# Kernel tuning notes

Measured on AMD Instinct MI355X. Metric: run time of the kernel, lower is better.

## Reference

```python
import jax, jax.numpy as jnp
import numpy as np

CAPACITY_FACTOR = 1.2


def setup_inputs() -> dict:
    key = jax.random.key(0)
    k1, k2, k3 = jax.random.split(key, 3)
    B, S, D, E = 8, 4096, 512, 16
    x = jax.random.normal(k1, (B, S, D), dtype=jnp.float32)
    switch_w = jax.random.normal(k2, (E, D), dtype=jnp.float32) * 0.02
    switch_b = jnp.zeros((E,), dtype=jnp.float32)
    expert_w = jax.random.normal(k3, (E, D, D), dtype=jnp.float32) * 0.02
    expert_b = jnp.zeros((E, D), dtype=jnp.float32)
    return {"x": x, "switch_w": switch_w, "switch_b": switch_b,
            "expert_w": expert_w, "expert_b": expert_b}


def reference(x, switch_w, switch_b, expert_w, expert_b):
    B, S, D = x.shape
    E = switch_w.shape[0]
    N = B * S
    xf = x.reshape(N, D)

    # Router: softmax over experts, top-1 route.
    logits = xf @ switch_w.T + switch_b            # [N, E]
    probs = jax.nn.softmax(logits, axis=-1)
    route_probs = jnp.max(probs, axis=-1)          # [N]
    routes = jnp.argmax(probs, axis=-1)            # [N] int

    # Position of each token within its expert's queue (token order).
    oh = jax.nn.one_hot(routes, E, dtype=jnp.int32)            # [N, E]
    pos = jnp.take_along_axis(jnp.cumsum(oh, axis=0), routes[:, None], axis=1)[:, 0] - 1  # [N]

    capacity = int(CAPACITY_FACTOR * N / E)        # static
    keep = pos < capacity                          # [N] bool; overflow tokens dropped

    # Dispatch: scatter kept tokens into [E, capacity, D] buffer.
    # Out-of-capacity positions are out-of-bounds and dropped by scatter semantics.
    buf = jnp.zeros((E, capacity, D), dtype=xf.dtype).at[routes, pos].set(xf)

    # Per-expert Linear (torch Linear: y = x @ W.T + b), as one grouped GEMM.
    y = jnp.einsum('ecd,efd->ecf', buf, expert_w) + expert_b[:, None, :]  # [E, C, D]

    # Combine: gather expert outputs back; dropped tokens pass through x.
    gathered = y[routes, jnp.minimum(pos, capacity - 1)]       # [N, D]
    out = jnp.where(keep[:, None], gathered, xf) * route_probs[:, None]
    return out.reshape(B, S, D)
```

## Files before the change

### kernel.cpp

```cpp
#include <hip/hip_runtime.h>
#include <math.h>

#define N_TOK 32768
#define DIM   512
#define NEXP  16
#define CAP   2457
#define CAPP  2464
#define NCHUNK 512

typedef __attribute__((ext_vector_type(8))) short   short8;
typedef __attribute__((ext_vector_type(4))) short   short4v;
typedef __attribute__((ext_vector_type(4))) float   floatx4;
typedef __attribute__((ext_vector_type(4))) unsigned uint4v;

__device__ __forceinline__ short f2bf(float f) {
  unsigned u = __builtin_bit_cast(unsigned, f);
  unsigned r = u + 0x7FFFu + ((u >> 16) & 1u);
  return (short)(r >> 16);
}
__device__ __forceinline__ float bf2f(short h) {
  return __builtin_bit_cast(float, ((unsigned)(unsigned short)h) << 16);
}

__device__ __forceinline__ unsigned cvt_pk(float a, float b) {
  unsigned r;
  asm("v_cvt_pk_bf16_f32 %0, %1, %2" : "=v"(r) : "v"(a), "v"(b));
  return r;
}
__device__ __forceinline__ float pklo(unsigned h) {
  return __builtin_bit_cast(float, h << 16);
}
__device__ __forceinline__ float pkhi(unsigned h) {
  return __builtin_bit_cast(float, h & 0xFFFF0000u);
}

#define LGP 17
__global__ __launch_bounds__(256) void router_k(
    const float* __restrict__ x, const float* __restrict__ sw,
    const float* __restrict__ sb, const float* __restrict__ ew,
    int* __restrict__ route, float* __restrict__ prob, int* __restrict__ hist,
    short* __restrict__ x_bf, short* __restrict__ w_bf) {
  __shared__ short swh[16][520];
  __shared__ short swl[16][520];
  __shared__ float lgt[64][LGP];
  __shared__ float sbs[NEXP];

  int tid = threadIdx.x;

  {
    const float4* src = (const float4*)ew;
    uint2* dst = (uint2*)w_bf;
    int base = blockIdx.x * 2048 + tid;
#pragma unroll
    for (int i = 0; i < 8; ++i) {
      float4 f = src[base + i * 256];
      uint2 s;
      s.x = cvt_pk(f.x, f.y);
      s.y = cvt_pk(f.z, f.w);
      dst[base + i * 256] = s;
    }
  }

  {
    int idx = tid;
#pragma unroll
    for (int i = 0; i < 8; ++i, idx += 256) {
      int e = idx >> 7, k4 = idx & 127;
      float4 f = ((const float4*)(sw + e * DIM))[k4];
      unsigned h0 = cvt_pk(f.x, f.y);
      unsigned h1 = cvt_pk(f.z, f.w);
      unsigned l0 = cvt_pk(f.x - pklo(h0), f.y - pkhi(h0));
      unsigned l1 = cvt_pk(f.z - pklo(h1), f.w - pkhi(h1));
      uint2 hv; hv.x = h0; hv.y = h1;
      uint2 lv; lv.x = l0; lv.y = l1;
      *(uint2*)&swh[e][k4 * 4] = hv;
      *(uint2*)&swl[e][k4 * 4] = lv;
    }
  }
  if (tid < NEXP) sbs[tid] = sb[tid];
  __syncthreads();

  int wv = tid >> 6, lane = tid & 63, q = lane >> 4, l16 = lane & 15;
  int row = blockIdx.x * 64 + wv * 16 + l16;
  const float* xr = x + (size_t)row * DIM;
  short* xbr = x_bf + (size_t)row * DIM;

  floatx4 acc = {};
#pragma unroll 4
  for (int kc = 0; kc < 16; ++kc) {
    int k0 = kc * 32 + q * 8;
    float4 f0 = *(const float4*)(xr + k0);
    float4 f1 = *(const float4*)(xr + k0 + 4);
    unsigned h0 = cvt_pk(f0.x, f0.y);
    unsigned h1 = cvt_pk(f0.z, f0.w);
    unsigned h2 = cvt_pk(f1.x, f1.y);
    unsigned h3 = cvt_pk(f1.z, f1.w);
    unsigned l0 = cvt_pk(f0.x - pklo(h0), f0.y - pkhi(h0));
    unsigned l1 = cvt_pk(f0.z - pklo(h1), f0.w - pkhi(h1));
    unsigned l2 = cvt_pk(f1.x - pklo(h2), f1.y - pkhi(h2));
    unsigned l3 = cvt_pk(f1.z - pklo(h3), f1.w - pkhi(h3));
    uint4v hp = {h0, h1, h2, h3};
    uint4v lp = {l0, l1, l2, l3};
    short8 hi = __builtin_bit_cast(short8, hp);
    short8 lo = __builtin_bit_cast(short8, lp);
    *(short8*)(xbr + k0) = hi;
    short8 bh = *(const short8*)&swh[l16][k0];
    short8 bl = *(const short8*)&swl[l16][k0];
    acc = __builtin_amdgcn_mfma_f32_16x16x32_bf16(hi, bh, acc, 0, 0, 0);
    acc = __builtin_amdgcn_mfma_f32_16x16x32_bf16(lo, bh, acc, 0, 0, 0);
    acc = __builtin_amdgcn_mfma_f32_16x16x32_bf16(hi, bl, acc, 0, 0, 0);
  }
#pragma unroll
  for (int r = 0; r < 4; ++r)
    lgt[wv * 16 + q * 4 + r][l16] = acc[r];
  __syncthreads();

  if (tid < 64) {
    int t = blockIdx.x * 64 + tid;
    float lg[NEXP];
#pragma unroll
    for (int e = 0; e < NEXP; ++e) lg[e] = lgt[tid][e] + sbs[e];
    int arg = 0; float mx = lg[0];
#pragma unroll
    for (int e = 1; e < NEXP; ++e)
      if (lg[e] > mx) { mx = lg[e]; arg = e; }
    float s = 0.f;
#pragma unroll
    for (int e = 0; e < NEXP; ++e) s += expf(lg[e] - mx);
    route[t] = arg;
    prob[t]  = 1.0f / s;
#pragma unroll
    for (int e = 0; e < NEXP; ++e) {
      unsigned long long m = __ballot(arg == e);
      if (tid == e) hist[blockIdx.x * NEXP + e] = __popcll(m);
    }
  }
}

__global__ __launch_bounds__(256) void pos_k(
    const int* __restrict__ route, const float* __restrict__ prob,
    const int* __restrict__ hist, const float* __restrict__ x,
    float* __restrict__ out, int* __restrict__ lists,
    int* __restrict__ counts) {
  __shared__ int part[16][NEXP];
  __shared__ int base_s[NEXP];
  __shared__ int wcnt[4][NEXP];
  int tid = threadIdx.x;
  int b = blockIdx.x;
  int c0 = b * 4;
  {
    int g = tid >> 4, e = tid & 15;
    int s = 0;
    for (int c = g; c < c0; c += 16) s += hist[c * NEXP + e];
    part[g][e] = s;
  }
  __syncthreads();
  if (tid < NEXP) {
    int s = 0;
#pragma unroll
    for (int gg = 0; gg < 16; ++gg) s += part[gg][tid];
    base_s[tid] = s;
  }
  int wv = tid >> 6, lane = tid & 63;
  int t = b * 256 + wv * 64 + lane;
  int r = route[t];
  unsigned long long lower = (1ull << lane) - 1ull;
  int rank = 0;
#pragma unroll
  for (int e = 0; e < NEXP; ++e) {
    unsigned long long m = __ballot(r == e);
    if (r == e) rank = __popcll(m & lower);
    if (lane == e) wcnt[wv][e] = __popcll(m);
  }
  __syncthreads();
  int pre = base_s[r];
  for (int w2 = 0; w2 < wv; ++w2) pre += wcnt[w2][r];
  int pos = pre + rank;
  if (pos < CAP) {
    lists[r * CAPP + pos] = t;
  } else {
    float p = prob[t];
    const float4* xr = (const float4*)(x + (size_t)t * DIM);
    float4* o = (float4*)(out + (size_t)t * DIM);
    for (int d = 0; d < DIM / 4; ++d) {
      float4 v = xr[d];
      v.x *= p; v.y *= p; v.z *= p; v.w *= p;
      o[d] = v;
    }
  }
  if (b == 127 && tid < NEXP)
    counts[tid] = base_s[tid] + wcnt[0][tid] + wcnt[1][tid]
                + wcnt[2][tid] + wcnt[3][tid];
}

#define BM 128
#define BN 128
#define BKS 64
#define TPE 80
#define NWG_G (TPE * NEXP)
#define CPX_G (NWG_G / 8)

__global__ __launch_bounds__(256, 3) void gemm_k(
    const short* __restrict__ x_bf, const short* __restrict__ w_bf,
    const float* __restrict__ eb, const int* __restrict__ lists,
    const int* __restrict__ counts, const float* __restrict__ prob,
    float* __restrict__ out) {
  int orig = blockIdx.x;
  int wgid = (orig & 7) * CPX_G + (orig >> 3);
  int e    = wgid / TPE;
  int rem  = wgid - e * TPE;
  int by   = rem >> 2;
  int bx   = rem & 3;

  int cnt = counts[e]; if (cnt > CAP) cnt = CAP;
  int row0 = by * BM;
  if (row0 >= cnt) return;
  int col0 = bx * BN;

  __shared__ short A_s[BM * BKS];
  __shared__ short B_s[BN * BKS];
  __shared__ int rowtok[BM];

  int tid = threadIdx.x;
  if (tid < BM) {
    int gr = row0 + tid;
    rowtok[tid] = (gr < cnt) ? lists[e * CAPP + gr] : 0;
  }
  __syncthreads();

  int wv = tid >> 6, lane = tid & 63;
  int q = lane >> 4, l16 = lane & 15;
  int wrow = (wv & 2) * 32, wcol = (wv & 1) * 64;

  int r_loc = lane >> 3, c = lane & 7;
  const short* ga[4]; short* la[4];
  const short* gb[4]; short* lb[4];
#pragma unroll
  for (int t4 = 0; t4 < 4; ++t4) {
    int row = wv * 32 + t4 * 8 + r_loc;
    int g = c ^ (row & 7);
    ga[t4] = x_bf + (size_t)rowtok[row] * DIM + g * 8;
    la[t4] = &A_s[(wv * 32 + t4 * 8) * BKS];
    gb[t4] = w_bf + (size_t)(e * DIM + col0 + row) * DIM + g * 8;
    lb[t4] = &B_s[(wv * 32 + t4 * 8) * BKS];
  }

  floatx4 acc[4][4] = {};

  for (int k0 = 0; k0 < DIM; k0 += BKS) {
#pragma unroll
    for (int t4 = 0; t4 < 4; ++t4)
      __builtin_amdgcn_global_load_lds(
          (const __attribute__((address_space(1))) void*)(ga[t4] + k0),
          (__attribute__((address_space(3))) void*)(la[t4]), 16, 0, 0);
#pragma unroll
    for (int t4 = 0; t4 < 4; ++t4)
      __builtin_amdgcn_global_load_lds(
          (const __attribute__((address_space(1))) void*)(gb[t4] + k0),
          (__attribute__((address_space(3))) void*)(lb[t4]), 16, 0, 0);
    __syncthreads();
#pragma unroll
    for (int kk = 0; kk < 2; ++kk) {
      short8 af[4], bfv[4];
      int ckbase = kk * 4 + q;
#pragma unroll
      for (int sm = 0; sm < 4; ++sm) {
        int row = wrow + sm * 16 + l16;
        int ph = ckbase ^ (row & 7);
        af[sm] = *(const short8*)&A_s[row * BKS + ph * 8];
      }
#pragma unroll
      for (int sn = 0; sn < 4; ++sn) {
        int row = wcol + sn * 16 + l16;
        int ph = ckbase ^ (row & 7);
        bfv[sn] = *(const short8*)&B_s[row * BKS + ph * 8];
      }
#pragma unroll
      for (int sm = 0; sm < 4; ++sm)
#pragma unroll
        for (int sn = 0; sn < 4; ++sn)
          acc[sm][sn] = __builtin_amdgcn_mfma_f32_16x16x32_bf16(
              af[sm], bfv[sn], acc[sm][sn], 0, 0, 0);
    }
    __syncthreads();
  }

#pragma unroll
  for (int sm = 0; sm < 4; ++sm) {
    int tt[4]; float pp[4]; int vld[4];
#pragma unroll
    for (int rg = 0; rg < 4; ++rg) {
      int rr = wrow + sm * 16 + q * 4 + rg;
      int gr = row0 + rr;
      vld[rg] = (gr < cnt);
      tt[rg]  = rowtok[rr];
      pp[rg]  = vld[rg] ? prob[tt[rg]] : 0.f;
    }
#pragma unroll
    for (int sn = 0; sn < 4; ++sn) {
      int col = col0 + wcol + sn * 16 + l16;
      float bias = eb[e * DIM + col];
#pragma unroll
      for (int rg = 0; rg < 4; ++rg)
        if (vld[rg])
          out[(size_t)tt[rg] * DIM + col] = (acc[sm][sn][rg] + bias) * pp[rg];
    }
  }
}

extern "C" void kernel_launch(void* const* d_in, const int* in_sizes, int n_in,
                              void* d_out, int out_size, void* d_ws, size_t ws_size,
                              hipStream_t stream) {
  const float* x  = (const float*)d_in[0];
  const float* sw = (const float*)d_in[1];
  const float* sb = (const float*)d_in[2];
  const float* ew = (const float*)d_in[3];
  const float* eb = (const float*)d_in[4];
  float* out = (float*)d_out;

  char* ws = (char*)d_ws;
  int*   route  = (int*)(ws + 0);
  float* prob   = (float*)(ws + 131072);
  int*   hist   = (int*)(ws + 262144);
  int*   counts = (int*)(ws + 327680);
  int*   lists  = (int*)(ws + 327744);
  short* x_bf   = (short*)(ws + (1 << 20));
  short* w_bf   = (short*)(ws + (1 << 20) + 33554432);

  hipLaunchKernelGGL(router_k, dim3(NCHUNK), dim3(256), 0, stream,
                     x, sw, sb, ew, route, prob, hist, x_bf, w_bf);
  hipLaunchKernelGGL(pos_k, dim3(128), dim3(256), 0, stream,
                     route, prob, hist, x, out, lists, counts);
  hipLaunchKernelGGL(gemm_k, dim3(NWG_G), dim3(256), 0, stream,
                     x_bf, w_bf, eb, lists, counts, prob, out);
}
```

Baseline: 184.2 us.

## Double-buffer GEMM LDS tiles with async global-to-LDS prefetch

Converts the expert GEMM main loop to use two LDS buffers for A and B. The next K tile is prefetched via global_load_lds while the current one is computed, and explicit vmcnt waits replace the full syncthreads barriers. The aim is to hide global load latency behind MFMA work. LDS use doubles and occupancy is relaxed from 3 to 2 blocks per CU, which lowers the number of waves available for latency hiding.

```diff
diff --git a/kernel.cpp b/kernel.cpp
--- a/kernel.cpp
+++ b/kernel.cpp
@@ -196,11 +196,55 @@
 #define BM 128
 #define BN 128
 #define BKS 64
+#define KSTEPS (DIM / BKS)
 #define TPE 80
 #define NWG_G (TPE * NEXP)
 #define CPX_G (NWG_G / 8)
 
-__global__ __launch_bounds__(256, 3) void gemm_k(
+#define GEMM_STAGE(b, k0)                                                     \
+  {                                                                           \
+    _Pragma("unroll")                                                         \
+    for (int t4 = 0; t4 < 4; ++t4)                                            \
+      __builtin_amdgcn_global_load_lds(                                       \
+          (const __attribute__((address_space(1))) void*)(ga[t4] + (k0)),     \
+          (__attribute__((address_space(3))) void*)(la[t4] + (b) * (BM*BKS)), \
+          16, 0, 0);                                                          \
+    _Pragma("unroll")                                                         \
+    for (int t4 = 0; t4 < 4; ++t4)                                            \
+      __builtin_amdgcn_global_load_lds(                                       \
+          (const __attribute__((address_space(1))) void*)(gb[t4] + (k0)),     \
+          (__attribute__((address_space(3))) void*)(lb[t4] + (b) * (BN*BKS)), \
+          16, 0, 0);                                                          \
+  }
+
+#define GEMM_COMPUTE(b)                                                       \
+  {                                                                           \
+    _Pragma("unroll")                                                         \
+    for (int kk = 0; kk < 2; ++kk) {                                          \
+      short8 af[4], bfv[4];                                                   \
+      int ckbase = kk * 4 + q;                                                \
+      _Pragma("unroll")                                                       \
+      for (int sm = 0; sm < 4; ++sm) {                                        \
+        int row = wrow + sm * 16 + l16;                                       \
+        int ph = ckbase ^ (row & 7);                                          \
+        af[sm] = *(const short8*)&A_s[b][row * BKS + ph * 8];                 \
+      }                                                                       \
+      _Pragma("unroll")                                                       \
+      for (int sn = 0; sn < 4; ++sn) {                                        \
+        int row = wcol + sn * 16 + l16;                                       \
+        int ph = ckbase ^ (row & 7);                                          \
+        bfv[sn] = *(const short8*)&B_s[b][row * BKS + ph * 8];                \
+      }                                                                       \
+      _Pragma("unroll")                                                       \
+      for (int sm = 0; sm < 4; ++sm)                                          \
+        _Pragma("unroll")                                                     \
+        for (int sn = 0; sn < 4; ++sn)                                        \
+          acc[sm][sn] = __builtin_amdgcn_mfma_f32_16x16x32_bf16(              \
+              af[sm], bfv[sn], acc[sm][sn], 0, 0, 0);                         \
+    }                                                                         \
+  }
+
+__global__ __launch_bounds__(256, 2) void gemm_k(
     const short* __restrict__ x_bf, const short* __restrict__ w_bf,
     const float* __restrict__ eb, const int* __restrict__ lists,
     const int* __restrict__ counts, const float* __restrict__ prob,
@@ -217,8 +261,8 @@
   if (row0 >= cnt) return;
   int col0 = bx * BN;
 
-  __shared__ short A_s[BM * BKS];
-  __shared__ short B_s[BN * BKS];
+  __shared__ short A_s[2][BM * BKS];
+  __shared__ short B_s[2][BN * BKS];
   __shared__ int rowtok[BM];
 
   int tid = threadIdx.x;
@@ -240,49 +284,28 @@
     int row = wv * 32 + t4 * 8 + r_loc;
     int g = c ^ (row & 7);
     ga[t4] = x_bf + (size_t)rowtok[row] * DIM + g * 8;
-    la[t4] = &A_s[(wv * 32 + t4 * 8) * BKS];
+    la[t4] = &A_s[0][(wv * 32 + t4 * 8) * BKS];
     gb[t4] = w_bf + (size_t)(e * DIM + col0 + row) * DIM + g * 8;
-    lb[t4] = &B_s[(wv * 32 + t4 * 8) * BKS];
+    lb[t4] = &B_s[0][(wv * 32 + t4 * 8) * BKS];
   }
 
   floatx4 acc[4][4] = {};
 
-  for (int k0 = 0; k0 < DIM; k0 += BKS) {
-#pragma unroll
-    for (int t4 = 0; t4 < 4; ++t4)
-      __builtin_amdgcn_global_load_lds(
-          (const __attribute__((address_space(1))) void*)(ga[t4] + k0),
-          (__attribute__((address_space(3))) void*)(la[t4]), 16, 0, 0);
-#pragma unroll
-    for (int t4 = 0; t4 < 4; ++t4)
-      __builtin_amdgcn_global_load_lds(
-          (const __attribute__((address_space(1))) void*)(gb[t4] + k0),
-          (__attribute__((address_space(3))) void*)(lb[t4]), 16, 0, 0);
-    __syncthreads();
-#pragma unroll
-    for (int kk = 0; kk < 2; ++kk) {
-      short8 af[4], bfv[4];
-      int ckbase = kk * 4 + q;
-#pragma unroll
-      for (int sm = 0; sm < 4; ++sm) {
-        int row = wrow + sm * 16 + l16;
-        int ph = ckbase ^ (row & 7);
-        af[sm] = *(const short8*)&A_s[row * BKS + ph * 8];
-      }
-#pragma unroll
-      for (int sn = 0; sn < 4; ++sn) {
-        int row = wcol + sn * 16 + l16;
-        int ph = ckbase ^ (row & 7);
-        bfv[sn] = *(const short8*)&B_s[row * BKS + ph * 8];
-      }
-#pragma unroll
-      for (int sm = 0; sm < 4; ++sm)
-#pragma unroll
-        for (int sn = 0; sn < 4; ++sn)
-          acc[sm][sn] = __builtin_amdgcn_mfma_f32_16x16x32_bf16(
-              af[sm], bfv[sn], acc[sm][sn], 0, 0, 0);
-    }
-    __syncthreads();
+  GEMM_STAGE(0, 0);
+  GEMM_STAGE(1, BKS);
+#pragma unroll
+  for (int k = 0; k < KSTEPS; ++k) {
+    if (k < KSTEPS - 1)
+      asm volatile("s_waitcnt vmcnt(8)" ::: "memory");
+    else
+      asm volatile("s_waitcnt vmcnt(0)" ::: "memory");
+    __builtin_amdgcn_s_barrier();
+    GEMM_COMPUTE(k & 1);
+    if (k < KSTEPS - 1) {
+      __builtin_amdgcn_s_barrier();
+      if (k + 2 < KSTEPS)
+        GEMM_STAGE(k & 1, (k + 2) * BKS);
+    }
   }
 
 #pragma unroll
```

Result: slower. 188.5 us (+2.4%).

## Split router K dimension across waves and drop LDS staging of switch weights

Applied to the files above, without the earlier changes.

The router kernel now processes 16 tokens per block across 2048 blocks instead of 64 tokens across 512, with each of the four waves handling a 128-wide slice of the K dimension and partial logits reduced through shared memory. Switch weights are converted to hi/lo bf16 directly into registers per wave instead of being staged through LDS with a block barrier. The intent is more parallelism and occupancy for the memory-bound router and cast pass, at the cost of each block re-reading switch weights, more histogram chunks for the position kernel to scan, and a cross-wave reduction.

```diff
diff --git a/kernel.cpp b/kernel.cpp
--- a/kernel.cpp
+++ b/kernel.cpp
@@ -6,22 +6,12 @@
 #define NEXP  16
 #define CAP   2457
 #define CAPP  2464
-#define NCHUNK 512
 
 typedef __attribute__((ext_vector_type(8))) short   short8;
 typedef __attribute__((ext_vector_type(4))) short   short4v;
 typedef __attribute__((ext_vector_type(4))) float   floatx4;
 typedef __attribute__((ext_vector_type(4))) unsigned uint4v;
 
-__device__ __forceinline__ short f2bf(float f) {
-  unsigned u = __builtin_bit_cast(unsigned, f);
-  unsigned r = u + 0x7FFFu + ((u >> 16) & 1u);
-  return (short)(r >> 16);
-}
-__device__ __forceinline__ float bf2f(short h) {
-  return __builtin_bit_cast(float, ((unsigned)(unsigned short)h) << 16);
-}
-
 __device__ __forceinline__ unsigned cvt_pk(float a, float b) {
   unsigned r;
   asm("v_cvt_pk_bf16_f32 %0, %1, %2" : "=v"(r) : "v"(a), "v"(b));
@@ -34,25 +24,25 @@
   return __builtin_bit_cast(float, h & 0xFFFF0000u);
 }
 
-#define LGP 17
-__global__ __launch_bounds__(256) void router_k(
+#define RTPB 16
+#define NRB  (N_TOK / RTPB)
+__global__ __launch_bounds__(256, 4) void router_k(
     const float* __restrict__ x, const float* __restrict__ sw,
     const float* __restrict__ sb, const float* __restrict__ ew,
     int* __restrict__ route, float* __restrict__ prob, int* __restrict__ hist,
     short* __restrict__ x_bf, short* __restrict__ w_bf) {
-  __shared__ short swh[16][520];
-  __shared__ short swl[16][520];
-  __shared__ float lgt[64][LGP];
+  __shared__ float plgt[4][16][17];
   __shared__ float sbs[NEXP];
 
   int tid = threadIdx.x;
+  int b = blockIdx.x;
 
   {
     const float4* src = (const float4*)ew;
     uint2* dst = (uint2*)w_bf;
-    int base = blockIdx.x * 2048 + tid;
-#pragma unroll
-    for (int i = 0; i < 8; ++i) {
+    int base = b * 512 + tid;
+#pragma unroll
+    for (int i = 0; i < 2; ++i) {
       float4 f = src[base + i * 256];
       uint2 s;
       s.x = cvt_pk(f.x, f.y);
@@ -60,66 +50,66 @@
       dst[base + i * 256] = s;
     }
   }
-
-  {
-    int idx = tid;
-#pragma unroll
-    for (int i = 0; i < 8; ++i, idx += 256) {
-      int e = idx >> 7, k4 = idx & 127;
-      float4 f = ((const float4*)(sw + e * DIM))[k4];
-      unsigned h0 = cvt_pk(f.x, f.y);
-      unsigned h1 = cvt_pk(f.z, f.w);
-      unsigned l0 = cvt_pk(f.x - pklo(h0), f.y - pkhi(h0));
-      unsigned l1 = cvt_pk(f.z - pklo(h1), f.w - pkhi(h1));
-      uint2 hv; hv.x = h0; hv.y = h1;
-      uint2 lv; lv.x = l0; lv.y = l1;
-      *(uint2*)&swh[e][k4 * 4] = hv;
-      *(uint2*)&swl[e][k4 * 4] = lv;
-    }
-  }
   if (tid < NEXP) sbs[tid] = sb[tid];
-  __syncthreads();
 
   int wv = tid >> 6, lane = tid & 63, q = lane >> 4, l16 = lane & 15;
-  int row = blockIdx.x * 64 + wv * 16 + l16;
-  const float* xr = x + (size_t)row * DIM;
-  short* xbr = x_bf + (size_t)row * DIM;
+  int row = b * RTPB + l16;
+  int kbase = wv * 128;
+  const float* xr  = x + (size_t)row * DIM + kbase;
+  short* xbr = x_bf + (size_t)row * DIM + kbase;
+  const float* swr = sw + (size_t)l16 * DIM + kbase;
+
+  short8 bh[4], bl[4];
+#pragma unroll
+  for (int kc = 0; kc < 4; ++kc) {
+    int k0 = kc * 32 + q * 8;
+    float4 f0 = *(const float4*)(swr + k0);
+    float4 f1 = *(const float4*)(swr + k0 + 4);
+    unsigned h0 = cvt_pk(f0.x, f0.y), h1 = cvt_pk(f0.z, f0.w);
+    unsigned h2 = cvt_pk(f1.x, f1.y), h3 = cvt_pk(f1.z, f1.w);
+    unsigned s0 = cvt_pk(f0.x - pklo(h0), f0.y - pkhi(h0));
+    unsigned s1 = cvt_pk(f0.z - pklo(h1), f0.w - pkhi(h1));
+    unsigned s2 = cvt_pk(f1.x - pklo(h2), f1.y - pkhi(h2));
+    unsigned s3 = cvt_pk(f1.z - pklo(h3), f1.w - pkhi(h3));
+    uint4v hp = {h0, h1, h2, h3};
+    uint4v lp = {s0, s1, s2, s3};
+    bh[kc] = __builtin_bit_cast(short8, hp);
+    bl[kc] = __builtin_bit_cast(short8, lp);
+  }
 
   floatx4 acc = {};
-#pragma unroll 4
-  for (int kc = 0; kc < 16; ++kc) {
+#pragma unroll
+  for (int kc = 0; kc < 4; ++kc) {
     int k0 = kc * 32 + q * 8;
     float4 f0 = *(const float4*)(xr + k0);
     float4 f1 = *(const float4*)(xr + k0 + 4);
-    unsigned h0 = cvt_pk(f0.x, f0.y);
-    unsigned h1 = cvt_pk(f0.z, f0.w);
-    unsigned h2 = cvt_pk(f1.x, f1.y);
-    unsigned h3 = cvt_pk(f1.z, f1.w);
-    unsigned l0 = cvt_pk(f0.x - pklo(h0), f0.y - pkhi(h0));
-    unsigned l1 = cvt_pk(f0.z - pklo(h1), f0.w - pkhi(h1));
-    unsigned l2 = cvt_pk(f1.x - pklo(h2), f1.y - pkhi(h2));
-    unsigned l3 = cvt_pk(f1.z - pklo(h3), f1.w - pkhi(h3));
+    unsigned h0 = cvt_pk(f0.x, f0.y), h1 = cvt_pk(f0.z, f0.w);
+    unsigned h2 = cvt_pk(f1.x, f1.y), h3 = cvt_pk(f1.z, f1.w);
+    unsigned s0 = cvt_pk(f0.x - pklo(h0), f0.y - pkhi(h0));
+    unsigned s1 = cvt_pk(f0.z - pklo(h1), f0.w - pkhi(h1));
+    unsigned s2 = cvt_pk(f1.x - pklo(h2), f1.y - pkhi(h2));
+    unsigned s3 = cvt_pk(f1.z - pklo(h3), f1.w - pkhi(h3));
     uint4v hp = {h0, h1, h2, h3};
-    uint4v lp = {l0, l1, l2, l3};
+    uint4v lp = {s0, s1, s2, s3};
     short8 hi = __builtin_bit_cast(short8, hp);
     short8 lo = __builtin_bit_cast(short8, lp);
     *(short8*)(xbr + k0) = hi;
-    short8 bh = *(const short8*)&swh[l16][k0];
-    short8 bl = *(const short8*)&swl[l16][k0];
-    acc = __builtin_amdgcn_mfma_f32_16x16x32_bf16(hi, bh, acc, 0, 0, 0);
-    acc = __builtin_amdgcn_mfma_f32_16x16x32_bf16(lo, bh, acc, 0, 0, 0);
-    acc = __builtin_amdgcn_mfma_f32_16x16x32_bf16(hi, bl, acc, 0, 0, 0);
+    acc = __builtin_amdgcn_mfma_f32_16x16x32_bf16(hi, bh[kc], acc, 0, 0, 0);
+    acc = __builtin_amdgcn_mfma_f32_16x16x32_bf16(lo, bh[kc], acc, 0, 0, 0);
+    acc = __builtin_amdgcn_mfma_f32_16x16x32_bf16(hi, bl[kc], acc, 0, 0, 0);
   }
 #pragma unroll
   for (int r = 0; r < 4; ++r)
-    lgt[wv * 16 + q * 4 + r][l16] = acc[r];
+    plgt[wv][q * 4 + r][l16] = acc[r];
   __syncthreads();
 
-  if (tid < 64) {
-    int t = blockIdx.x * 64 + tid;
+  if (tid < RTPB) {
+    int t = b * RTPB + tid;
     float lg[NEXP];
 #pragma unroll
-    for (int e = 0; e < NEXP; ++e) lg[e] = lgt[tid][e] + sbs[e];
+    for (int e = 0; e < NEXP; ++e)
+      lg[e] = plgt[0][tid][e] + plgt[1][tid][e] + plgt[2][tid][e]
+            + plgt[3][tid][e] + sbs[e];
     int arg = 0; float mx = lg[0];
 #pragma unroll
     for (int e = 1; e < NEXP; ++e)
@@ -132,7 +122,7 @@
 #pragma unroll
     for (int e = 0; e < NEXP; ++e) {
       unsigned long long m = __ballot(arg == e);
-      if (tid == e) hist[blockIdx.x * NEXP + e] = __popcll(m);
+      if (tid == e) hist[b * NEXP + e] = __popcll(m);
     }
   }
 }
@@ -147,7 +137,7 @@
   __shared__ int wcnt[4][NEXP];
   int tid = threadIdx.x;
   int b = blockIdx.x;
-  int c0 = b * 4;
+  int c0 = b * 16;
   {
     int g = tid >> 4, e = tid & 15;
     int s = 0;
@@ -322,12 +312,12 @@
   int*   route  = (int*)(ws + 0);
   float* prob   = (float*)(ws + 131072);
   int*   hist   = (int*)(ws + 262144);
-  int*   counts = (int*)(ws + 327680);
-  int*   lists  = (int*)(ws + 327744);
+  int*   counts = (int*)(ws + 393216);
+  int*   lists  = (int*)(ws + 393280);
   short* x_bf   = (short*)(ws + (1 << 20));
   short* w_bf   = (short*)(ws + (1 << 20) + 33554432);
 
-  hipLaunchKernelGGL(router_k, dim3(NCHUNK), dim3(256), 0, stream,
+  hipLaunchKernelGGL(router_k, dim3(NRB), dim3(256), 0, stream,
                      x, sw, sb, ew, route, prob, hist, x_bf, w_bf);
   hipLaunchKernelGGL(pos_k, dim3(128), dim3(256), 0, stream,
                      route, prob, hist, x, out, lists, counts);
```

After: 198.6 us. 1.08x slower.
